# Kernel tuning notes

Measured on AMD Instinct MI355X. Metric: run time of the kernel, lower is better.

## Reference

```python
import jax, jax.numpy as jnp
import numpy as np

N_NODES = 100000
N_EDGES = 1000000
IN_CH = 128
OUT_CH = 128
T_DIM = 64


def setup_inputs() -> dict:
    key = jax.random.key(0)
    ks = jax.random.split(key, 9)
    x = jax.random.normal(ks[0], (N_NODES, IN_CH), dtype=jnp.float32)
    edge_index = jax.random.randint(ks[1], (2, N_EDGES), 0, N_NODES, dtype=jnp.int64)
    temporal_features = jax.random.normal(ks[2], (N_EDGES, T_DIM), dtype=jnp.float32)
    # Learned params (torch nn.Linear convention: weight [out, in], bias [out])
    s = 1.0 / np.sqrt(IN_CH)
    st = 1.0 / np.sqrt(T_DIM)
    W_S_w = jax.random.uniform(ks[3], (OUT_CH, IN_CH), minval=-s, maxval=s, dtype=jnp.float32)
    W_S_b = jax.random.uniform(ks[4], (OUT_CH,), minval=-s, maxval=s, dtype=jnp.float32)
    W_T_w = jax.random.uniform(ks[5], (OUT_CH, IN_CH), minval=-s, maxval=s, dtype=jnp.float32)
    W_T_b = jax.random.uniform(ks[6], (OUT_CH,), minval=-s, maxval=s, dtype=jnp.float32)
    T_w = jax.random.uniform(ks[7], (OUT_CH, T_DIM), minval=-st, maxval=st, dtype=jnp.float32)
    T_b = jax.random.uniform(ks[8], (OUT_CH,), minval=-st, maxval=st, dtype=jnp.float32)
    return {
        "x": x, "edge_index": edge_index, "temporal_features": temporal_features,
        "W_S_w": W_S_w, "W_S_b": W_S_b, "W_T_w": W_T_w, "W_T_b": W_T_b,
        "T_w": T_w, "T_b": T_b,
    }


def reference(x, edge_index, temporal_features, W_S_w, W_S_b, W_T_w, W_T_b, T_w, T_b):
    num_nodes = x.shape[0]
    row, col = edge_index[0], edge_index[1]
    # self transform: [N, out]
    self_features = x @ W_S_w.T + W_S_b
    # gather neighbor feats then transform: [E, out]
    neighbor_features = x[col] @ W_T_w.T + W_T_b
    # temporal encodings: [E, out]
    temporal_encodings = temporal_features @ T_w.T + T_b
    messages = neighbor_features + temporal_encodings
    # scatter-add aggregation over destination nodes
    aggregated = jax.ops.segment_sum(messages, row, num_segments=num_nodes)
    return jax.nn.relu(self_features + aggregated)
```

## Files before the change

kernel.cpp:

```cpp
#include <hip/hip_runtime.h>

#define N_NODES 100000
#define M_PAD   100096
#define N_EDGES 1000000
#define K_TOT   320
#define NCHUNK  98

#define BM  128
#define LDA 72

#define XCONV_THREADS 1600000
#define PREP_BLOCKS   6410
#define HIST_BLOCKS   3907

typedef __attribute__((ext_vector_type(8))) short bf16x8;
typedef __attribute__((ext_vector_type(4))) float f32x4;

__device__ __forceinline__ unsigned short f2bf(float f) {
    unsigned u = __float_as_uint(f);
    u += 0x7FFFu + ((u >> 16) & 1u);
    return (unsigned short)(u >> 16);
}
__device__ __forceinline__ unsigned pack2(float a, float b) {
    return (unsigned)f2bf(a) | ((unsigned)f2bf(b) << 16);
}
__device__ __forceinline__ float bflo(unsigned v) { return __uint_as_float(v << 16); }
__device__ __forceinline__ float bfhi(unsigned v) { return __uint_as_float(v & 0xffff0000u); }

__global__ __launch_bounds__(256) void prep_hist_kernel(
        const float* __restrict__ x,
        const float* __restrict__ WSw,
        const float* __restrict__ WTw,
        const float* __restrict__ Tw,
        const float* __restrict__ WTb,
        const float* __restrict__ Tb,
        unsigned short* __restrict__ xb,
        unsigned short* __restrict__ Gtb,
        float* __restrict__ bias2,
        const int* __restrict__ ei,
        int* __restrict__ hist) {
    int b = blockIdx.x;
    int t = threadIdx.x;
    if (b >= PREP_BLOCKS) {
        int e = (b - PREP_BLOCKS) * 256 + t;
        if (e < N_EDGES) atomicAdd(&hist[ei[e]], 1);
        return;
    }
    int gid = b * 256 + t;
    if (gid < XCONV_THREADS) {
        const float4* p = (const float4*)x + (size_t)gid * 2;
        float4 u0 = p[0], u1 = p[1];
        uint4 w;
        w.x = pack2(u0.x, u0.y);
        w.y = pack2(u0.z, u0.w);
        w.z = pack2(u1.x, u1.y);
        w.w = pack2(u1.z, u1.w);
        *(uint4*)(xb + (size_t)gid * 8) = w;
    } else {
        int idx = gid - XCONV_THREADS;
        if (idx < K_TOT * 128) {
            int k = idx >> 7;
            int o = idx & 127;
            float v = (k < 128) ? WSw[o * 128 + k]
                    : (k < 256) ? WTw[o * 128 + (k - 128)]
                                : Tw[o * 64 + (k - 256)];
            Gtb[(size_t)o * K_TOT + k] = f2bf(v);
        }
        if (idx < 128) bias2[idx] = WTb[idx] + Tb[idx];
    }
}

__global__ __launch_bounds__(256) void scan_pass1(const int* __restrict__ hist,
                                                  int* __restrict__ chunksum) {
    __shared__ int ts[256];
    int b = blockIdx.x, t = threadIdx.x;
    int i = b * 1024 + t * 4;
    int s = 0;
#pragma unroll
    for (int j = 0; j < 4; ++j)
        if (i + j < N_NODES) s += hist[i + j];
    ts[t] = s;
    __syncthreads();
    for (int off = 128; off > 0; off >>= 1) {
        if (t < off) ts[t] += ts[t + off];
        __syncthreads();
    }
    if (t == 0) chunksum[b] = ts[0];
}

__global__ __launch_bounds__(128) void scan_mid(const int* __restrict__ chunksum,
                                                int* __restrict__ chunkoff) {
    __shared__ int ts[128];
    int t = threadIdx.x;
    int v = (t < NCHUNK) ? chunksum[t] : 0;
    ts[t] = v;
    __syncthreads();
    for (int off = 1; off < 128; off <<= 1) {
        int a = (t >= off) ? ts[t - off] : 0;
        __syncthreads();
        ts[t] += a;
        __syncthreads();
    }
    if (t < NCHUNK) chunkoff[t] = ts[t] - v;
}

__global__ __launch_bounds__(256) void scan_pass2(const int* __restrict__ hist,
                                                  const int* __restrict__ chunkoff,
                                                  int* __restrict__ offsets) {
    __shared__ int ts[256];
    int b = blockIdx.x, t = threadIdx.x;
    int i0 = b * 1024 + t * 4;
    int v[4];
    int s = 0;
#pragma unroll
    for (int j = 0; j < 4; ++j) {
        v[j] = (i0 + j < N_NODES) ? hist[i0 + j] : 0;
        s += v[j];
    }
    ts[t] = s;
    __syncthreads();
    for (int off = 1; off < 256; off <<= 1) {
        int add = (t >= off) ? ts[t - off] : 0;
        __syncthreads();
        ts[t] += add;
        __syncthreads();
    }
    int run = chunkoff[b] + ts[t] - s;
#pragma unroll
    for (int j = 0; j < 4; ++j) {
        if (i0 + j < N_NODES) offsets[i0 + j] = run;
        run += v[j];
    }
}

__global__ __launch_bounds__(256) void fill_kernel(const int* __restrict__ ei,
                                                   int* __restrict__ offsets,
                                                   unsigned long long* __restrict__ ec) {
    int e = blockIdx.x * 256 + threadIdx.x;
    if (e < N_EDGES) {
        int row = ei[e];
        int col = ei[N_EDGES + e];
        int pos = atomicAdd(&offsets[row], 1);
        ec[pos] = ((unsigned long long)(unsigned)col << 32) | (unsigned)e;
    }
}

__global__ __launch_bounds__(256) void agg_kernel(
        const unsigned* __restrict__ xw,
        const float* __restrict__ tf,
        const unsigned long long* __restrict__ ec,
        const int* __restrict__ offsets,
        unsigned* __restrict__ aggxb,
        unsigned* __restrict__ aggtb,
        float* __restrict__ deg) {
    int lane = threadIdx.x & 63;
    int n = blockIdx.x * 4 + (threadIdx.x >> 6);

    int beg = n ? offsets[n - 1] : 0;
    int end = offsets[n];

    float ax = 0.f, ay = 0.f, at = 0.f;
    float bx = 0.f, by = 0.f, bt = 0.f;

    int i = beg;
    for (; i + 3 < end; i += 4) {
        unsigned long long p0 = ec[i],     p1 = ec[i + 1];
        unsigned long long p2 = ec[i + 2], p3 = ec[i + 3];
        unsigned a = xw[((size_t)(p0 >> 32) << 6) + lane];
        unsigned b = xw[((size_t)(p1 >> 32) << 6) + lane];
        unsigned c = xw[((size_t)(p2 >> 32) << 6) + lane];
        unsigned d = xw[((size_t)(p3 >> 32) << 6) + lane];
        float u0 = __builtin_nontemporal_load(tf + ((size_t)(unsigned)p0 << 6) + lane);
        float u1 = __builtin_nontemporal_load(tf + ((size_t)(unsigned)p1 << 6) + lane);
        float u2 = __builtin_nontemporal_load(tf + ((size_t)(unsigned)p2 << 6) + lane);
        float u3 = __builtin_nontemporal_load(tf + ((size_t)(unsigned)p3 << 6) + lane);
        ax += bflo(a); ay += bfhi(a); at += u0;
        bx += bflo(b); by += bfhi(b); bt += u1;
        ax += bflo(c); ay += bfhi(c); at += u2;
        bx += bflo(d); by += bfhi(d); bt += u3;
    }
    int rem = end - i;
    if (rem) {
        unsigned long long p0 = ec[i];
        unsigned long long p1 = (rem > 1) ? ec[i + 1] : p0;
        unsigned long long p2 = (rem > 2) ? ec[i + 2] : p0;
        unsigned a = xw[((size_t)(p0 >> 32) << 6) + lane];
        unsigned b = xw[((size_t)(p1 >> 32) << 6) + lane];
        unsigned c = xw[((size_t)(p2 >> 32) << 6) + lane];
        float u0 = __builtin_nontemporal_load(tf + ((size_t)(unsigned)p0 << 6) + lane);
        float u1 = __builtin_nontemporal_load(tf + ((size_t)(unsigned)p1 << 6) + lane);
        float u2 = __builtin_nontemporal_load(tf + ((size_t)(unsigned)p2 << 6) + lane);
        ax += bflo(a); ay += bfhi(a); at += u0;
        if (rem > 1) { bx += bflo(b); by += bfhi(b); bt += u1; }
        if (rem > 2) { ax += bflo(c); ay += bfhi(c); at += u2; }
    }

    float fx = ax + bx, fy = ay + by, ft = at + bt;
    aggxb[(size_t)n * 64 + lane] = pack2(fx, fy);
    float pt = __shfl_xor(ft, 1);
    if (!(lane & 1))
        aggtb[(size_t)n * 32 + (lane >> 1)] = pack2(ft, pt);
    if (lane == 0) deg[n] = (float)(end - beg);
}

__global__ __launch_bounds__(256) void gemm_kernel(
        const unsigned short* __restrict__ xb,
        const unsigned short* __restrict__ aggxb,
        const unsigned short* __restrict__ aggtb,
        const unsigned short* __restrict__ Gtb,
        const float* __restrict__ WSb,
        const float* __restrict__ bias2,
        const float* __restrict__ deg,
        float* __restrict__ out) {
    __shared__ unsigned short As[BM * LDA];
    __shared__ unsigned short Bs[BM * LDA];

    int t = threadIdx.x;
    int lane = t & 63;
    int wave = t >> 6;
    int mw = (wave & 1) * 64;
    int nw = (wave >> 1) * 64;
    int row0 = blockIdx.x * BM;
    int quad = lane >> 4;
    int l16  = lane & 15;

    f32x4 acc[4][4];
#pragma unroll
    for (int mt = 0; mt < 4; ++mt)
#pragma unroll
        for (int nt = 0; nt < 4; ++nt)
            acc[mt][nt] = (f32x4){0.f, 0.f, 0.f, 0.f};

    int sm = t >> 1;
    int sh = (t & 1) * 32;

    for (int c = 0; c < 5; ++c) {
        const unsigned short* src; int ld, koff;
        if (c < 2)      { src = xb;    ld = 128; koff = c * 64; }
        else if (c < 4) { src = aggxb; ld = 128; koff = (c - 2) * 64; }
        else            { src = aggtb; ld = 64;  koff = 0; }

        const unsigned short* ap = src + (size_t)(row0 + sm) * ld + koff + sh;
        uint4 a0 = *(const uint4*)(ap);
        uint4 a1 = *(const uint4*)(ap + 8);
        uint4 a2 = *(const uint4*)(ap + 16);
        uint4 a3 = *(const uint4*)(ap + 24);
        const unsigned short* gp = Gtb + (size_t)sm * K_TOT + c * 64 + sh;
        uint4 b0 = *(const uint4*)(gp);
        uint4 b1 = *(const uint4*)(gp + 8);
        uint4 b2 = *(const uint4*)(gp + 16);
        uint4 b3 = *(const uint4*)(gp + 24);

        __syncthreads();

        *(uint4*)&As[sm * LDA + sh]      = a0;
        *(uint4*)&As[sm * LDA + sh + 8]  = a1;
        *(uint4*)&As[sm * LDA + sh + 16] = a2;
        *(uint4*)&As[sm * LDA + sh + 24] = a3;
        *(uint4*)&Bs[sm * LDA + sh]      = b0;
        *(uint4*)&Bs[sm * LDA + sh + 8]  = b1;
        *(uint4*)&Bs[sm * LDA + sh + 16] = b2;
        *(uint4*)&Bs[sm * LDA + sh + 24] = b3;

        __syncthreads();

#pragma unroll
        for (int ks = 0; ks < 2; ++ks) {
            bf16x8 af[4], bfv[4];
#pragma unroll
            for (int mt = 0; mt < 4; ++mt)
                af[mt] = *(bf16x8*)&As[(mw + mt * 16 + l16) * LDA + ks * 32 + quad * 8];
#pragma unroll
            for (int nt = 0; nt < 4; ++nt)
                bfv[nt] = *(bf16x8*)&Bs[(nw + nt * 16 + l16) * LDA + ks * 32 + quad * 8];
#pragma unroll
            for (int mt = 0; mt < 4; ++mt)
#pragma unroll
                for (int nt = 0; nt < 4; ++nt)
                    acc[mt][nt] = __builtin_amdgcn_mfma_f32_16x16x32_bf16(
                        af[mt], bfv[nt], acc[mt][nt], 0, 0, 0);
        }
    }

#pragma unroll
    for (int mt = 0; mt < 4; ++mt) {
#pragma unroll
        for (int r = 0; r < 4; ++r) {
            int m = row0 + mw + mt * 16 + quad * 4 + r;
            if (m >= N_NODES) continue;
            float dg = deg[m];
#pragma unroll
            for (int nt = 0; nt < 4; ++nt) {
                int o = nw + nt * 16 + l16;
                float val = acc[mt][nt][r] + WSb[o] + dg * bias2[o];
                out[(size_t)m * 128 + o] = fmaxf(val, 0.f);
            }
        }
    }
}

extern "C" void kernel_launch(void* const* d_in, const int* in_sizes, int n_in,
                              void* d_out, int out_size, void* d_ws, size_t ws_size,
                              hipStream_t stream) {
    const float* x   = (const float*)d_in[0];
    const int*   ei  = (const int*)d_in[1];
    const float* tf  = (const float*)d_in[2];
    const float* WSw = (const float*)d_in[3];
    const float* WSb = (const float*)d_in[4];
    const float* WTw = (const float*)d_in[5];
    const float* WTb = (const float*)d_in[6];
    const float* Tw  = (const float*)d_in[7];
    const float* Tb  = (const float*)d_in[8];
    float* out = (float*)d_out;

    unsigned short* xb    = (unsigned short*)d_ws;
    unsigned short* aggxb = xb    + (size_t)M_PAD * 128;
    unsigned short* aggtb = aggxb + (size_t)M_PAD * 128;
    unsigned short* Gtb   = aggtb + (size_t)M_PAD * 64;
    unsigned long long* ec = (unsigned long long*)(Gtb + (size_t)K_TOT * 128);
    float* deg   = (float*)(ec + N_EDGES);
    float* bias2 = deg + N_NODES;
    int* hist    = (int*)(bias2 + 128);
    int* offsets = hist + N_NODES;
    int* csum    = offsets + (N_NODES + 2);
    int* coff    = csum + 128;

    hipMemsetAsync(hist, 0, (size_t)N_NODES * sizeof(int), stream);

    prep_hist_kernel<<<PREP_BLOCKS + HIST_BLOCKS, 256, 0, stream>>>(
        x, WSw, WTw, Tw, WTb, Tb, xb, Gtb, bias2, ei, hist);

    scan_pass1<<<NCHUNK, 256, 0, stream>>>(hist, csum);
    scan_mid<<<1, 128, 0, stream>>>(csum, coff);
    scan_pass2<<<NCHUNK, 256, 0, stream>>>(hist, coff, offsets);

    fill_kernel<<<(N_EDGES + 255) / 256, 256, 0, stream>>>(ei, offsets, ec);

    agg_kernel<<<N_NODES / 4, 256, 0, stream>>>(
        (const unsigned*)xb, tf, ec, offsets, (unsigned*)aggxb, (unsigned*)aggtb, deg);

    gemm_kernel<<<(N_NODES + BM - 1) / BM, 256, 0, stream>>>(
        xb, aggxb, aggtb, Gtb, WSb, bias2, deg, out);
}
```

Before: 575.9 us.

## Fold scan_mid into pass2, deepen gather unroll, use direct-to-LDS swizzled GEMM loads

Removes the single-block scan_mid launch: each scan_pass2 block sums the preceding chunk sums itself with a wave reduction. The aggregation kernel now keeps eight gathers in flight per iteration with four partial accumulators, handling the tail by clamping indices, to raise memory-level parallelism. The GEMM stages its A and B tiles with global_load_lds into an XOR-swizzled unpadded layout, hoists the bias loads and uses nontemporal output stores. These changes target launch overhead, gather latency and register-staged LDS copies, at the cost of redundant tail loads and more complex addressing.

```diff
diff --git a/kernel.cpp b/kernel.cpp
--- a/kernel.cpp
+++ b/kernel.cpp
@@ -7,7 +7,6 @@
 #define NCHUNK  98
 
 #define BM  128
-#define LDA 72
 
 #define XCONV_THREADS 1600000
 #define PREP_BLOCKS   6410
@@ -26,6 +25,12 @@
 }
 __device__ __forceinline__ float bflo(unsigned v) { return __uint_as_float(v << 16); }
 __device__ __forceinline__ float bfhi(unsigned v) { return __uint_as_float(v & 0xffff0000u); }
+
+__device__ __forceinline__ void gl_lds16(const void* g, void* l) {
+    __builtin_amdgcn_global_load_lds(
+        (const __attribute__((address_space(1))) unsigned*)g,
+        (__attribute__((address_space(3))) unsigned*)l, 16, 0, 0);
+}
 
 __global__ __launch_bounds__(256) void prep_hist_kernel(
         const float* __restrict__ x,
@@ -88,26 +93,11 @@
     if (t == 0) chunksum[b] = ts[0];
 }
 
-__global__ __launch_bounds__(128) void scan_mid(const int* __restrict__ chunksum,
-                                                int* __restrict__ chunkoff) {
-    __shared__ int ts[128];
-    int t = threadIdx.x;
-    int v = (t < NCHUNK) ? chunksum[t] : 0;
-    ts[t] = v;
-    __syncthreads();
-    for (int off = 1; off < 128; off <<= 1) {
-        int a = (t >= off) ? ts[t - off] : 0;
-        __syncthreads();
-        ts[t] += a;
-        __syncthreads();
-    }
-    if (t < NCHUNK) chunkoff[t] = ts[t] - v;
-}
-
 __global__ __launch_bounds__(256) void scan_pass2(const int* __restrict__ hist,
-                                                  const int* __restrict__ chunkoff,
+                                                  const int* __restrict__ csum,
                                                   int* __restrict__ offsets) {
     __shared__ int ts[256];
+    __shared__ int cbase_s;
     int b = blockIdx.x, t = threadIdx.x;
     int i0 = b * 1024 + t * 4;
     int v[4];
@@ -118,6 +108,12 @@
         s += v[j];
     }
     ts[t] = s;
+    if (t < 64) {
+        int cs = 0;
+        for (int i = t; i < b; i += 64) cs += csum[i];
+        for (int off = 32; off; off >>= 1) cs += __shfl_down(cs, off);
+        if (t == 0) cbase_s = cs;
+    }
     __syncthreads();
     for (int off = 1; off < 256; off <<= 1) {
         int add = (t >= off) ? ts[t - off] : 0;
@@ -125,7 +121,7 @@
         ts[t] += add;
         __syncthreads();
     }
-    int run = chunkoff[b] + ts[t] - s;
+    int run = cbase_s + ts[t] - s;
 #pragma unroll
     for (int j = 0; j < 4; ++j) {
         if (i0 + j < N_NODES) offsets[i0 + j] = run;
@@ -159,43 +155,61 @@
     int beg = n ? offsets[n - 1] : 0;
     int end = offsets[n];
 
-    float ax = 0.f, ay = 0.f, at = 0.f;
-    float bx = 0.f, by = 0.f, bt = 0.f;
+    float ax[4] = {0.f, 0.f, 0.f, 0.f};
+    float ay[4] = {0.f, 0.f, 0.f, 0.f};
+    float at[4] = {0.f, 0.f, 0.f, 0.f};
 
     int i = beg;
-    for (; i + 3 < end; i += 4) {
-        unsigned long long p0 = ec[i],     p1 = ec[i + 1];
-        unsigned long long p2 = ec[i + 2], p3 = ec[i + 3];
-        unsigned a = xw[((size_t)(p0 >> 32) << 6) + lane];
-        unsigned b = xw[((size_t)(p1 >> 32) << 6) + lane];
-        unsigned c = xw[((size_t)(p2 >> 32) << 6) + lane];
-        unsigned d = xw[((size_t)(p3 >> 32) << 6) + lane];
-        float u0 = __builtin_nontemporal_load(tf + ((size_t)(unsigned)p0 << 6) + lane);
-        float u1 = __builtin_nontemporal_load(tf + ((size_t)(unsigned)p1 << 6) + lane);
-        float u2 = __builtin_nontemporal_load(tf + ((size_t)(unsigned)p2 << 6) + lane);
-        float u3 = __builtin_nontemporal_load(tf + ((size_t)(unsigned)p3 << 6) + lane);
-        ax += bflo(a); ay += bfhi(a); at += u0;
-        bx += bflo(b); by += bfhi(b); bt += u1;
-        ax += bflo(c); ay += bfhi(c); at += u2;
-        bx += bflo(d); by += bfhi(d); bt += u3;
+    for (; i + 7 < end; i += 8) {
+        unsigned long long p[8];
+#pragma unroll
+        for (int j = 0; j < 8; ++j) p[j] = ec[i + j];
+        unsigned xv[8];
+        float tv[8];
+#pragma unroll
+        for (int j = 0; j < 8; ++j)
+            xv[j] = xw[((size_t)(p[j] >> 32) << 6) + lane];
+#pragma unroll
+        for (int j = 0; j < 8; ++j)
+            tv[j] = __builtin_nontemporal_load(tf + ((size_t)(unsigned)p[j] << 6) + lane);
+#pragma unroll
+        for (int j = 0; j < 8; ++j) {
+            ax[j & 3] += bflo(xv[j]);
+            ay[j & 3] += bfhi(xv[j]);
+            at[j & 3] += tv[j];
+        }
     }
     int rem = end - i;
     if (rem) {
-        unsigned long long p0 = ec[i];
-        unsigned long long p1 = (rem > 1) ? ec[i + 1] : p0;
-        unsigned long long p2 = (rem > 2) ? ec[i + 2] : p0;
-        unsigned a = xw[((size_t)(p0 >> 32) << 6) + lane];
-        unsigned b = xw[((size_t)(p1 >> 32) << 6) + lane];
-        unsigned c = xw[((size_t)(p2 >> 32) << 6) + lane];
-        float u0 = __builtin_nontemporal_load(tf + ((size_t)(unsigned)p0 << 6) + lane);
-        float u1 = __builtin_nontemporal_load(tf + ((size_t)(unsigned)p1 << 6) + lane);
-        float u2 = __builtin_nontemporal_load(tf + ((size_t)(unsigned)p2 << 6) + lane);
-        ax += bflo(a); ay += bfhi(a); at += u0;
-        if (rem > 1) { bx += bflo(b); by += bfhi(b); bt += u1; }
-        if (rem > 2) { ax += bflo(c); ay += bfhi(c); at += u2; }
-    }
-
-    float fx = ax + bx, fy = ay + by, ft = at + bt;
+        int last = end - 1;
+        unsigned long long p[8];
+#pragma unroll
+        for (int j = 0; j < 8; ++j) {
+            int idx = i + j;
+            if (idx > last) idx = last;
+            p[j] = ec[idx];
+        }
+        unsigned xv[8];
+        float tv[8];
+#pragma unroll
+        for (int j = 0; j < 8; ++j)
+            xv[j] = xw[((size_t)(p[j] >> 32) << 6) + lane];
+#pragma unroll
+        for (int j = 0; j < 8; ++j)
+            tv[j] = __builtin_nontemporal_load(tf + ((size_t)(unsigned)p[j] << 6) + lane);
+#pragma unroll
+        for (int j = 0; j < 8; ++j) {
+            if (j < rem) {
+                ax[j & 3] += bflo(xv[j]);
+                ay[j & 3] += bfhi(xv[j]);
+                at[j & 3] += tv[j];
+            }
+        }
+    }
+
+    float fx = (ax[0] + ax[1]) + (ax[2] + ax[3]);
+    float fy = (ay[0] + ay[1]) + (ay[2] + ay[3]);
+    float ft = (at[0] + at[1]) + (at[2] + at[3]);
     aggxb[(size_t)n * 64 + lane] = pack2(fx, fy);
     float pt = __shfl_xor(ft, 1);
     if (!(lane & 1))
@@ -212,8 +226,8 @@
         const float* __restrict__ bias2,
         const float* __restrict__ deg,
         float* __restrict__ out) {
-    __shared__ unsigned short As[BM * LDA];
-    __shared__ unsigned short Bs[BM * LDA];
+    __shared__ unsigned short As[BM * 64];
+    __shared__ unsigned short Bs[BM * 64];
 
     int t = threadIdx.x;
     int lane = t & 63;
@@ -224,6 +238,10 @@
     int quad = lane >> 4;
     int l16  = lane & 15;
 
+    int lr = lane >> 3;
+    int lc = lane & 7;
+    int swz = ((lc ^ lr) << 4);
+
     f32x4 acc[4][4];
 #pragma unroll
     for (int mt = 0; mt < 4; ++mt)
@@ -231,48 +249,34 @@
         for (int nt = 0; nt < 4; ++nt)
             acc[mt][nt] = (f32x4){0.f, 0.f, 0.f, 0.f};
 
-    int sm = t >> 1;
-    int sh = (t & 1) * 32;
-
     for (int c = 0; c < 5; ++c) {
-        const unsigned short* src; int ld, koff;
-        if (c < 2)      { src = xb;    ld = 128; koff = c * 64; }
-        else if (c < 4) { src = aggxb; ld = 128; koff = (c - 2) * 64; }
-        else            { src = aggtb; ld = 64;  koff = 0; }
-
-        const unsigned short* ap = src + (size_t)(row0 + sm) * ld + koff + sh;
-        uint4 a0 = *(const uint4*)(ap);
-        uint4 a1 = *(const uint4*)(ap + 8);
-        uint4 a2 = *(const uint4*)(ap + 16);
-        uint4 a3 = *(const uint4*)(ap + 24);
-        const unsigned short* gp = Gtb + (size_t)sm * K_TOT + c * 64 + sh;
-        uint4 b0 = *(const uint4*)(gp);
-        uint4 b1 = *(const uint4*)(gp + 8);
-        uint4 b2 = *(const uint4*)(gp + 16);
-        uint4 b3 = *(const uint4*)(gp + 24);
-
-        __syncthreads();
-
-        *(uint4*)&As[sm * LDA + sh]      = a0;
-        *(uint4*)&As[sm * LDA + sh + 8]  = a1;
-        *(uint4*)&As[sm * LDA + sh + 16] = a2;
-        *(uint4*)&As[sm * LDA + sh + 24] = a3;
-        *(uint4*)&Bs[sm * LDA + sh]      = b0;
-        *(uint4*)&Bs[sm * LDA + sh + 8]  = b1;
-        *(uint4*)&Bs[sm * LDA + sh + 16] = b2;
-        *(uint4*)&Bs[sm * LDA + sh + 24] = b3;
-
+        const char* srcA; size_t ldb, koffb;
+        if (c < 2)      { srcA = (const char*)xb;    ldb = 256; koffb = (size_t)c * 128; }
+        else if (c < 4) { srcA = (const char*)aggxb; ldb = 256; koffb = (size_t)(c - 2) * 128; }
+        else            { srcA = (const char*)aggtb; ldb = 128; koffb = 0; }
+
+        __syncthreads();
+#pragma unroll
+        for (int j = 0; j < 4; ++j) {
+            int r = wave * 4 + j;
+            int row = r * 8 + lr;
+            gl_lds16(srcA + (size_t)(row0 + row) * ldb + koffb + swz,
+                     (char*)As + r * 1024);
+            gl_lds16((const char*)Gtb + (size_t)row * 640 + (size_t)c * 128 + swz,
+                     (char*)Bs + r * 1024);
+        }
         __syncthreads();
 
 #pragma unroll
         for (int ks = 0; ks < 2; ++ks) {
             bf16x8 af[4], bfv[4];
+            int rb = ((ks * 64 + quad * 16) ^ ((l16 & 7) << 4));
 #pragma unroll
             for (int mt = 0; mt < 4; ++mt)
-                af[mt] = *(bf16x8*)&As[(mw + mt * 16 + l16) * LDA + ks * 32 + quad * 8];
+                af[mt] = *(const bf16x8*)((const char*)As + (mw + mt * 16 + l16) * 128 + rb);
 #pragma unroll
             for (int nt = 0; nt < 4; ++nt)
-                bfv[nt] = *(bf16x8*)&Bs[(nw + nt * 16 + l16) * LDA + ks * 32 + quad * 8];
+                bfv[nt] = *(const bf16x8*)((const char*)Bs + (nw + nt * 16 + l16) * 128 + rb);
 #pragma unroll
             for (int mt = 0; mt < 4; ++mt)
 #pragma unroll
@@ -282,6 +286,13 @@
         }
     }
 
+    float wsb[4], b2[4];
+#pragma unroll
+    for (int nt = 0; nt < 4; ++nt) {
+        int o = nw + nt * 16 + l16;
+        wsb[nt] = WSb[o];
+        b2[nt]  = bias2[o];
+    }
 #pragma unroll
     for (int mt = 0; mt < 4; ++mt) {
 #pragma unroll
@@ -292,8 +303,8 @@
 #pragma unroll
             for (int nt = 0; nt < 4; ++nt) {
                 int o = nw + nt * 16 + l16;
-                float val = acc[mt][nt][r] + WSb[o] + dg * bias2[o];
-                out[(size_t)m * 128 + o] = fmaxf(val, 0.f);
+                float val = acc[mt][nt][r] + wsb[nt] + dg * b2[nt];
+                __builtin_nontemporal_store(fmaxf(val, 0.f), &out[(size_t)m * 128 + o]);
             }
         }
     }
@@ -323,7 +334,6 @@
     int* hist    = (int*)(bias2 + 128);
     int* offsets = hist + N_NODES;
     int* csum    = offsets + (N_NODES + 2);
-    int* coff    = csum + 128;
 
     hipMemsetAsync(hist, 0, (size_t)N_NODES * sizeof(int), stream);
 
@@ -331,8 +341,7 @@
         x, WSw, WTw, Tw, WTb, Tb, xb, Gtb, bias2, ei, hist);
 
     scan_pass1<<<NCHUNK, 256, 0, stream>>>(hist, csum);
-    scan_mid<<<1, 128, 0, stream>>>(csum, coff);
-    scan_pass2<<<NCHUNK, 256, 0, stream>>>(hist, coff, offsets);
+    scan_pass2<<<NCHUNK, 256, 0, stream>>>(hist, csum, offsets);
 
     fill_kernel<<<(N_EDGES + 255) / 256, 256, 0, stream>>>(ei, offsets, ec);
 
```

Result: no change. 575.4 us (-0.1%).
